# Performance work log

Hardware: AMD Instinct MI355X
Metric: run time of the kernel (lower is better)

Reference implementation:

```python
import jax, jax.numpy as jnp
import numpy as np

N = 100000
E = 1600000
D = 128


def setup_inputs() -> dict:
    key = jax.random.key(0)
    k1, k2, k3, k4, k5 = jax.random.split(key, 5)
    x = jax.random.normal(k1, (N, D), dtype=jnp.float32)
    edge_row = jax.random.randint(k2, (E,), 0, N, dtype=jnp.int32)
    edge_col = jax.random.randint(k3, (E,), 0, N, dtype=jnp.int32)
    edge_weight = jax.random.uniform(k4, (E,), dtype=jnp.float32)
    # xavier_uniform for square weight: limit = sqrt(6/(fan_in+fan_out))
    limit = float(np.sqrt(6.0 / (D + D)))
    W = jax.random.uniform(k5, (D, D), dtype=jnp.float32, minval=-limit, maxval=limit)
    b = jnp.zeros((D,), dtype=jnp.float32)
    return {"x": x, "edge_row": edge_row, "edge_col": edge_col,
            "edge_weight": edge_weight, "W": W, "b": b}


def reference(x, edge_row, edge_col, edge_weight, W, b):
    # res = x (in_features == out_features -> res_linear is None)
    h = jnp.dot(x, W.T) + b                      # [N, D] dense linear
    msgs = h[edge_col] * edge_weight[:, None]    # [E, D] gather + scale (spmm)
    agg = jax.ops.segment_sum(msgs, edge_row, num_segments=N)  # [N, D] scatter-add
    return jax.nn.leaky_relu(agg + x, negative_slope=0.2)
```

## Files before the change

### kernel.cpp

```cpp
#include <hip/hip_runtime.h>

#define DIM 128
#define SB_SHIFT 9
#define SB_ROWS 512
#define SBCAP 10240
#define TILE1 4096

typedef short bf16x8 __attribute__((ext_vector_type(8)));
typedef float f32x4  __attribute__((ext_vector_type(4)));

__device__ inline unsigned int f2b(float f) {
  unsigned int u = __float_as_uint(f);
  unsigned int r = u + 0x7FFFu + ((u >> 16) & 1u);
  return r >> 16;
}
__device__ inline unsigned int f2b2(float lo, float hi) {
  return f2b(lo) | (f2b(hi) << 16);
}
__device__ inline void cvt8(const float* __restrict__ src, unsigned short* dst,
                            size_t i8) {
  const float4* xp = reinterpret_cast<const float4*>(src) + i8 * 2;
  float4 a = xp[0], c = xp[1];
  uint4 o;
  o.x = f2b2(a.x, a.y);
  o.y = f2b2(a.z, a.w);
  o.z = f2b2(c.x, c.y);
  o.w = f2b2(c.z, c.w);
  reinterpret_cast<uint4*>(dst)[i8] = o;
}
__device__ inline unsigned int q4(float a, float b, float c, float d, float inv) {
  int qa = (int)rintf(a * inv), qb = (int)rintf(b * inv);
  int qc = (int)rintf(c * inv), qd = (int)rintf(d * inv);
  return ((unsigned int)(qa & 255)) | ((unsigned int)(qb & 255) << 8) |
         ((unsigned int)(qc & 255) << 16) | ((unsigned int)(qd & 255) << 24);
}

__global__ __launch_bounds__(256) void prep_all(
    const float* __restrict__ W, unsigned short* __restrict__ Wb,
    const float* __restrict__ x, unsigned short* __restrict__ xb,
    unsigned int* __restrict__ xq, float* __restrict__ scale,
    int* __restrict__ cnt, int nelem8, int ncw, int nxb) {
  const int bid = (int)blockIdx.x;
  const int t = threadIdx.x;
  if (bid < ncw) {
    int i = bid * 256 + t;
    if (i < DIM * DIM / 8) cvt8(W, Wb, i);
    return;
  }
  if (bid == ncw + nxb) {
#pragma unroll
    for (int k = 0; k < 4; ++k) cnt[t * 4 + k] = 0;
    return;
  }
  int i = (bid - ncw) * 256 + t;
  if (i >= nelem8) return;

  const float4* xp = reinterpret_cast<const float4*>(x) + (size_t)i * 2;
  float4 a = xp[0], c = xp[1];

  uint4 o;
  o.x = f2b2(a.x, a.y);
  o.y = f2b2(a.z, a.w);
  o.z = f2b2(c.x, c.y);
  o.w = f2b2(c.z, c.w);
  reinterpret_cast<uint4*>(xb)[i] = o;

  float m = fmaxf(fmaxf(fmaxf(fabsf(a.x), fabsf(a.y)), fmaxf(fabsf(a.z), fabsf(a.w))),
                  fmaxf(fmaxf(fabsf(c.x), fabsf(c.y)), fmaxf(fabsf(c.z), fabsf(c.w))));
#pragma unroll
  for (int d = 1; d < 16; d <<= 1) m = fmaxf(m, __shfl_xor(m, d));

  float inv = (m > 0.f) ? 127.f / m : 0.f;
  uint2 q;
  q.x = q4(a.x, a.y, a.z, a.w, inv);
  q.y = q4(c.x, c.y, c.z, c.w, inv);
  reinterpret_cast<uint2*>(xq)[i] = q;
  if ((t & 15) == 0) scale[i >> 4] = (m > 0.f) ? m / 127.f : 0.f;
}

__global__ __launch_bounds__(256) void part1(
    const int* __restrict__ erow, const int* __restrict__ ecol,
    const float* __restrict__ ew, int* __restrict__ cnt,
    int2* __restrict__ gL1, int E, int NSB) {
  __shared__ int2 stage[TILE1];
  __shared__ unsigned short sbid[TILE1];
  __shared__ int lcnt[256], loff[256], gbs[256], stmp[256];

  const int t = threadIdx.x;
  const int base = blockIdx.x * TILE1;
  const int ntile = min(TILE1, E - base);

  lcnt[t] = 0;
  __syncthreads();

  int rk[TILE1 / 256];
#pragma unroll
  for (int i = 0; i < TILE1 / 256; ++i) {
    int e = base + t + i * 256;
    rk[i] = -1;
    if (e < E) {
      int bkt = erow[e] >> SB_SHIFT;
      rk[i] = atomicAdd(&lcnt[bkt], 1);
    }
  }
  __syncthreads();

  int myc = lcnt[t];
  stmp[t] = myc;
  __syncthreads();
  for (int d = 1; d < 256; d <<= 1) {
    int val = (t >= d) ? stmp[t - d] : 0;
    __syncthreads();
    stmp[t] += val;
    __syncthreads();
  }
  loff[t] = stmp[t] - myc;
  if (t < NSB && myc > 0) gbs[t] = atomicAdd(&cnt[t], myc);
  __syncthreads();

#pragma unroll
  for (int i = 0; i < TILE1 / 256; ++i) {
    int e = base + t + i * 256;
    if (e < E) {
      int row = erow[e];
      int bkt = row >> SB_SHIFT;
      int slot = loff[bkt] + rk[i];
      int wq = (int)(ew[e] * 32768.f + 0.5f);
      wq = min(wq, 32767);
      stage[slot] = make_int2(((row & (SB_ROWS - 1)) << 17) | ecol[e], wq);
      sbid[slot] = (unsigned short)bkt;
    }
  }
  __syncthreads();

  for (int s = t; s < ntile; s += 256) {
    int bkt = sbid[s];
    int rel = gbs[bkt] + (s - loff[bkt]);
    if (rel < SBCAP)
      gL1[(size_t)bkt * SBCAP + rel] = stage[s];
  }
}

__global__ __launch_bounds__(512) void part2(
    const int2* __restrict__ gL1, const int* __restrict__ cnt,
    int* __restrict__ off, int* __restrict__ deg,
    unsigned int* __restrict__ sedge, int N) {
  __shared__ int hist[SB_ROWS];
  __shared__ int scn[SB_ROWS];
  __shared__ int cur[SB_ROWS];
  const int t = threadIdx.x;
  const int srow = blockIdx.x << SB_SHIFT;
  const int start = blockIdx.x * SBCAP;
  const int end = start + min(cnt[blockIdx.x], SBCAP);

  hist[t] = 0;
  __syncthreads();
  for (int i = start + t; i < end; i += 512)
    atomicAdd(&hist[((unsigned)gL1[i].x) >> 17], 1);
  __syncthreads();

  int v = hist[t];
  scn[t] = v;
  __syncthreads();
  for (int d = 1; d < SB_ROWS; d <<= 1) {
    int val = (t >= d) ? scn[t - d] : 0;
    __syncthreads();
    scn[t] += val;
    __syncthreads();
  }
  int o = start + scn[t] - v;
  cur[t] = o;
  int row = srow + t;
  if (row < N) {
    off[row] = o;
    deg[row] = v;
  }
  __syncthreads();

  for (int i = start + t; i < end; i += 512) {
    int2 p = gL1[i];
    int rowlo = ((unsigned)p.x) >> 17;
    int dst = atomicAdd(&cur[rowlo], 1);
    sedge[dst] = ((unsigned int)p.x & 0x1FFFFu) | ((unsigned int)p.y << 17);
  }
}

__global__ __launch_bounds__(256) void aggregate2(
    const unsigned int* __restrict__ xq, const float* __restrict__ scale,
    const int* __restrict__ off, const int* __restrict__ deg,
    const unsigned int* __restrict__ sedge,
    unsigned short* __restrict__ g, int N) {
  const int r = (blockIdx.x * 256 + threadIdx.x) >> 3;
  const int l = threadIdx.x & 7;
  if (r >= N) return;

  const int start = off[r];
  const int n = deg[r];

  float acc[16];
#pragma unroll
  for (int i = 0; i < 16; ++i) acc[i] = 0.f;

#define GATHER(pp) (*reinterpret_cast<const uint4*>(xq + (size_t)((pp) & 0x1FFFFu) * 32 + l * 4))
#define FEDGE(pp) ((float)((pp) >> 17) * (1.0f / 32768.f) * scale[(pp) & 0x1FFFFu])
#define ACC4(w_, qw, base)                                                 \
  {                                                                        \
    acc[base + 0] += w_ * (float)(signed char)((qw));                      \
    acc[base + 1] += w_ * (float)(signed char)((qw) >> 8);                 \
    acc[base + 2] += w_ * (float)(signed char)((qw) >> 16);                \
    acc[base + 3] += w_ * (float)(signed char)((qw) >> 24);                \
  }
#define ACCUM(qv, fv)                                                      \
  {                                                                        \
    float f_ = (fv);                                                       \
    ACC4(f_, (qv).x, 0);                                                   \
    ACC4(f_, (qv).y, 4);                                                   \
    ACC4(f_, (qv).z, 8);                                                   \
    ACC4(f_, (qv).w, 12);                                                  \
  }

  int j = 0;
  for (; j + 4 <= n; j += 4) {
    unsigned int p0 = sedge[start + j];
    unsigned int p1 = sedge[start + j + 1];
    unsigned int p2 = sedge[start + j + 2];
    unsigned int p3 = sedge[start + j + 3];
    uint4 h0 = GATHER(p0);
    uint4 h1 = GATHER(p1);
    uint4 h2 = GATHER(p2);
    uint4 h3 = GATHER(p3);
    float f0 = FEDGE(p0);
    float f1 = FEDGE(p1);
    float f2 = FEDGE(p2);
    float f3 = FEDGE(p3);
    ACCUM(h0, f0);
    ACCUM(h1, f1);
    ACCUM(h2, f2);
    ACCUM(h3, f3);
  }
  for (; j < n; ++j) {
    unsigned int p = sedge[start + j];
    uint4 hv = GATHER(p);
    ACCUM(hv, FEDGE(p));
  }
#undef GATHER
#undef FEDGE
#undef ACC4
#undef ACCUM

  uint4 o0, o1;
  o0.x = f2b2(acc[0], acc[1]);
  o0.y = f2b2(acc[2], acc[3]);
  o0.z = f2b2(acc[4], acc[5]);
  o0.w = f2b2(acc[6], acc[7]);
  o1.x = f2b2(acc[8], acc[9]);
  o1.y = f2b2(acc[10], acc[11]);
  o1.z = f2b2(acc[12], acc[13]);
  o1.w = f2b2(acc[14], acc[15]);
  uint4* gp = reinterpret_cast<uint4*>(g + (size_t)r * DIM + l * 16);
  gp[0] = o0;
  gp[1] = o1;
}

__global__ __launch_bounds__(256) void gemm2(
    const unsigned short* __restrict__ g, const unsigned short* __restrict__ Wb,
    const float* __restrict__ b, const unsigned short* __restrict__ xbr,
    float* __restrict__ out, int N) {
  __shared__ unsigned short Ws[DIM * DIM];

  const int t = threadIdx.x;
#pragma unroll
  for (int i = 0; i < 8; ++i) {
    int idx = i * 256 + t;
    int row = idx >> 4;
    int slot = idx & 15;
    uint4 v = reinterpret_cast<const uint4*>(Wb)[idx];
    reinterpret_cast<uint4*>(Ws)[row * 16 + (slot ^ (row & 7))] = v;
  }
  __syncthreads();

  const int wid  = t >> 6;
  const int lane = t & 63;
  const int m0   = blockIdx.x * 64 + wid * 16;
  const int mrow = m0 + (lane & 15);
  const int koff = (lane >> 4) * 8;
  const int arow = (mrow < N) ? mrow : N - 1;

  f32x4 acc[8];
#pragma unroll
  for (int j = 0; j < 8; ++j) acc[j] = (f32x4){0.f, 0.f, 0.f, 0.f};

#pragma unroll
  for (int k0 = 0; k0 < DIM; k0 += 32) {
    bf16x8 af = *reinterpret_cast<const bf16x8*>(g + (size_t)arow * DIM + k0 + koff);
    const int slotbase = (k0 >> 3) + (lane >> 4);
#pragma unroll
    for (int j = 0; j < 8; ++j) {
      int row = j * 16 + (lane & 15);
      const uint4* wp = reinterpret_cast<const uint4*>(Ws) +
                        row * 16 + (slotbase ^ (row & 7));
      bf16x8 bf = *reinterpret_cast<const bf16x8*>(wp);
      acc[j] = __builtin_amdgcn_mfma_f32_16x16x32_bf16(af, bf, acc[j], 0, 0, 0);
    }
  }

  const int rowbase = (lane >> 4) * 4;
#pragma unroll
  for (int j = 0; j < 8; ++j) {
    int n = j * 16 + (lane & 15);
    float bias = b[n];
#pragma unroll
    for (int i = 0; i < 4; ++i) {
      int m = m0 + rowbase + i;
      if (m < N) {
        float res = __uint_as_float((unsigned int)xbr[(size_t)m * DIM + n] << 16);
        float v = acc[j][i] + bias + res;
        out[(size_t)m * DIM + n] = v > 0.f ? v : 0.2f * v;
      }
    }
  }
}

extern "C" void kernel_launch(void* const* d_in, const int* in_sizes, int n_in,
                              void* d_out, int out_size, void* d_ws,
                              size_t ws_size, hipStream_t stream) {
  const float* x  = (const float*)d_in[0];
  const int* erow = (const int*)d_in[1];
  const int* ecol = (const int*)d_in[2];
  const float* ew = (const float*)d_in[3];
  const float* W  = (const float*)d_in[4];
  const float* b  = (const float*)d_in[5];
  float* out      = (float*)d_out;

  const int N = in_sizes[0] / DIM;
  const int E = in_sizes[1];
  const int NSB = (N + SB_ROWS - 1) >> SB_SHIFT;
  const int netile = (E + TILE1 - 1) / TILE1;

  char* wsp = (char*)d_ws;
  unsigned short* xb = (unsigned short*)wsp;  wsp += (size_t)N * DIM * sizeof(unsigned short);
  unsigned int* xq   = (unsigned int*)wsp;    wsp += (size_t)N * DIM;
  float* scale = (float*)wsp;                 wsp += (size_t)N * sizeof(float);
  unsigned short* g  = (unsigned short*)wsp;  wsp += (size_t)N * DIM * sizeof(unsigned short);
  int*   off   = (int*)wsp;                   wsp += (size_t)N * sizeof(int);
  int*   deg   = (int*)wsp;                   wsp += (size_t)N * sizeof(int);
  int*   cnt   = (int*)wsp;                   wsp += 4096;
  unsigned short* Wb = (unsigned short*)wsp;  wsp += DIM * DIM * sizeof(unsigned short);
  int2*  gL1   = (int2*)wsp;                  wsp += (size_t)NSB * SBCAP * sizeof(int2);
  unsigned int* sedge = (unsigned int*)wsp;   wsp += (size_t)NSB * SBCAP * sizeof(unsigned int);

  const int nelem8 = N * DIM / 8;
  const int ncw = (DIM * DIM / 8 + 255) / 256;
  const int nxb = (nelem8 + 255) / 256;
  prep_all<<<ncw + nxb + 1, 256, 0, stream>>>(W, Wb, x, xb, xq, scale, cnt,
                                              nelem8, ncw, nxb);

  part1<<<netile, 256, 0, stream>>>(erow, ecol, ew, cnt, gL1, E, NSB);

  part2<<<NSB, 512, 0, stream>>>(gL1, cnt, off, deg, sedge, N);

  aggregate2<<<(N + 31) / 32, 256, 0, stream>>>(xq, scale, off, deg, sedge, g, N);

  gemm2<<<(N + 63) / 64, 256, 0, stream>>>(g, Wb, b, xb, out, N);
}
```

Baseline: 119.0 us.

## Reuse int8-quantized x for residual and drop bf16 copy of x

Removes the bf16 copy of x written in the prep kernel and read back in the GEMM epilogue. The residual is now dequantized from the existing int8 per-row-scaled buffer. This cuts a full N×D write and read of memory traffic, at the cost of lower residual precision. The partition kernel part1 also moves from 256 to 512 threads per block.

```diff
diff --git a/kernel.cpp b/kernel.cpp
--- a/kernel.cpp
+++ b/kernel.cpp
@@ -37,7 +37,7 @@
 
 __global__ __launch_bounds__(256) void prep_all(
     const float* __restrict__ W, unsigned short* __restrict__ Wb,
-    const float* __restrict__ x, unsigned short* __restrict__ xb,
+    const float* __restrict__ x,
     unsigned int* __restrict__ xq, float* __restrict__ scale,
     int* __restrict__ cnt, int nelem8, int ncw, int nxb) {
   const int bid = (int)blockIdx.x;
@@ -58,13 +58,6 @@
   const float4* xp = reinterpret_cast<const float4*>(x) + (size_t)i * 2;
   float4 a = xp[0], c = xp[1];
 
-  uint4 o;
-  o.x = f2b2(a.x, a.y);
-  o.y = f2b2(a.z, a.w);
-  o.z = f2b2(c.x, c.y);
-  o.w = f2b2(c.z, c.w);
-  reinterpret_cast<uint4*>(xb)[i] = o;
-
   float m = fmaxf(fmaxf(fmaxf(fabsf(a.x), fabsf(a.y)), fmaxf(fabsf(a.z), fabsf(a.w))),
                   fmaxf(fmaxf(fabsf(c.x), fabsf(c.y)), fmaxf(fabsf(c.z), fabsf(c.w))));
 #pragma unroll
@@ -78,7 +71,7 @@
   if ((t & 15) == 0) scale[i >> 4] = (m > 0.f) ? m / 127.f : 0.f;
 }
 
-__global__ __launch_bounds__(256) void part1(
+__global__ __launch_bounds__(512) void part1(
     const int* __restrict__ erow, const int* __restrict__ ecol,
     const float* __restrict__ ew, int* __restrict__ cnt,
     int2* __restrict__ gL1, int E, int NSB) {
@@ -90,13 +83,13 @@
   const int base = blockIdx.x * TILE1;
   const int ntile = min(TILE1, E - base);
 
-  lcnt[t] = 0;
-  __syncthreads();
-
-  int rk[TILE1 / 256];
-#pragma unroll
-  for (int i = 0; i < TILE1 / 256; ++i) {
-    int e = base + t + i * 256;
+  if (t < 256) lcnt[t] = 0;
+  __syncthreads();
+
+  int rk[TILE1 / 512];
+#pragma unroll
+  for (int i = 0; i < TILE1 / 512; ++i) {
+    int e = base + t + i * 512;
     rk[i] = -1;
     if (e < E) {
       int bkt = erow[e] >> SB_SHIFT;
@@ -105,22 +98,23 @@
   }
   __syncthreads();
 
-  int myc = lcnt[t];
-  stmp[t] = myc;
+  int myc = (t < 256) ? lcnt[t] : 0;
+  if (t < 256) stmp[t] = myc;
   __syncthreads();
   for (int d = 1; d < 256; d <<= 1) {
-    int val = (t >= d) ? stmp[t - d] : 0;
+    int val = 0;
+    if (t < 256 && t >= d) val = stmp[t - d];
     __syncthreads();
-    stmp[t] += val;
+    if (t < 256) stmp[t] += val;
     __syncthreads();
   }
-  loff[t] = stmp[t] - myc;
+  if (t < 256) loff[t] = stmp[t] - myc;
   if (t < NSB && myc > 0) gbs[t] = atomicAdd(&cnt[t], myc);
   __syncthreads();
 
 #pragma unroll
-  for (int i = 0; i < TILE1 / 256; ++i) {
-    int e = base + t + i * 256;
+  for (int i = 0; i < TILE1 / 512; ++i) {
+    int e = base + t + i * 512;
     if (e < E) {
       int row = erow[e];
       int bkt = row >> SB_SHIFT;
@@ -133,7 +127,7 @@
   }
   __syncthreads();
 
-  for (int s = t; s < ntile; s += 256) {
+  for (int s = t; s < ntile; s += 512) {
     int bkt = sbid[s];
     int rel = gbs[bkt] + (s - loff[bkt]);
     if (rel < SBCAP)
@@ -264,8 +258,8 @@
 
 __global__ __launch_bounds__(256) void gemm2(
     const unsigned short* __restrict__ g, const unsigned short* __restrict__ Wb,
-    const float* __restrict__ b, const unsigned short* __restrict__ xbr,
-    float* __restrict__ out, int N) {
+    const float* __restrict__ b, const unsigned int* __restrict__ xq,
+    const float* __restrict__ scale, float* __restrict__ out, int N) {
   __shared__ unsigned short Ws[DIM * DIM];
 
   const int t = threadIdx.x;
@@ -305,6 +299,12 @@
   }
 
   const int rowbase = (lane >> 4) * 4;
+  float sq[4];
+#pragma unroll
+  for (int i = 0; i < 4; ++i) {
+    int m = m0 + rowbase + i;
+    sq[i] = (m < N) ? scale[m] : 0.f;
+  }
 #pragma unroll
   for (int j = 0; j < 8; ++j) {
     int n = j * 16 + (lane & 15);
@@ -313,7 +313,8 @@
     for (int i = 0; i < 4; ++i) {
       int m = m0 + rowbase + i;
       if (m < N) {
-        float res = __uint_as_float((unsigned int)xbr[(size_t)m * DIM + n] << 16);
+        unsigned int w = xq[(size_t)m * 32 + (n >> 2)];
+        float res = (float)(signed char)(w >> ((n & 3) * 8)) * sq[i];
         float v = acc[j][i] + bias + res;
         out[(size_t)m * DIM + n] = v > 0.f ? v : 0.2f * v;
       }
@@ -338,7 +339,6 @@
   const int netile = (E + TILE1 - 1) / TILE1;
 
   char* wsp = (char*)d_ws;
-  unsigned short* xb = (unsigned short*)wsp;  wsp += (size_t)N * DIM * sizeof(unsigned short);
   unsigned int* xq   = (unsigned int*)wsp;    wsp += (size_t)N * DIM;
   float* scale = (float*)wsp;                 wsp += (size_t)N * sizeof(float);
   unsigned short* g  = (unsigned short*)wsp;  wsp += (size_t)N * DIM * sizeof(unsigned short);
@@ -352,14 +352,14 @@
   const int nelem8 = N * DIM / 8;
   const int ncw = (DIM * DIM / 8 + 255) / 256;
   const int nxb = (nelem8 + 255) / 256;
-  prep_all<<<ncw + nxb + 1, 256, 0, stream>>>(W, Wb, x, xb, xq, scale, cnt,
+  prep_all<<<ncw + nxb + 1, 256, 0, stream>>>(W, Wb, x, xq, scale, cnt,
                                               nelem8, ncw, nxb);
 
-  part1<<<netile, 256, 0, stream>>>(erow, ecol, ew, cnt, gL1, E, NSB);
+  part1<<<netile, 512, 0, stream>>>(erow, ecol, ew, cnt, gL1, E, NSB);
 
   part2<<<NSB, 512, 0, stream>>>(gL1, cnt, off, deg, sedge, N);
 
   aggregate2<<<(N + 31) / 32, 256, 0, stream>>>(xq, scale, off, deg, sedge, g, N);
 
-  gemm2<<<(N + 63) / 64, 256, 0, stream>>>(g, Wb, b, xb, out, N);
-}
+  gemm2<<<(N + 63) / 64, 256, 0, stream>>>(g, Wb, b, xq, scale, out, N);
+}
```

Measured after the change: 108.1 us. 9.2% less time.
